# Kernel tuning notes

Hardware: AMD Instinct MI355X
Metric: run time of the kernel (lower is better)

## Reference

```python
import jax, jax.numpy as jnp
import numpy as np
import math

BATCH, DIM, T, WIDTH = 4096, 100, 101, 200

def setup_inputs() -> dict:
    key = jax.random.key(0)
    ks = jax.random.split(key, 12)
    def lin(k, nin, nout):
        bound = 1.0 / math.sqrt(nin)
        kw, kb = jax.random.split(k)
        W = jax.random.uniform(kw, (nin, nout), jnp.float32, -bound, bound)
        b = jax.random.uniform(kb, (nout,), jnp.float32, -bound, bound)
        return W, b
    W0, b0 = lin(ks[0], DIM + 1, WIDTH)
    W1, b1 = lin(ks[1], WIDTH, WIDTH)
    W2, b2 = lin(ks[2], WIDTH, WIDTH)
    W3, b3 = lin(ks[3], WIDTH, WIDTH)
    Wout, bout = lin(ks[4], WIDTH, DIM)
    S0 = jax.random.normal(ks[5], (BATCH, DIM), jnp.float32)
    # standard-normal increments; scaled by sqrt(h) inside reference (matches torch randn * sqrt(h))
    dW = jax.random.normal(ks[6], (BATCH, DIM * T), jnp.float32)
    timegrid = jnp.linspace(0.0, 1.0, T, dtype=jnp.float32)
    return {"S0": S0, "timegrid": timegrid, "dW": dW,
            "W0": W0, "b0": b0, "W1": W1, "b1": b1, "W2": W2, "b2": b2,
            "W3": W3, "b3": b3, "Wout": Wout, "bout": bout}

def _mlp(x, W0, b0, W1, b1, W2, b2, W3, b3, Wout, bout):
    h = jax.nn.relu(x @ W0 + b0)
    h = jax.nn.relu(h @ W1 + b1)
    h = jax.nn.relu(h @ W2 + b2)
    h = jax.nn.relu(h @ W3 + b3)
    return h @ Wout + bout

def reference(S0, timegrid, dW, W0, b0, W1, b1, W2, b2, W3, b3, Wout, bout):
    B, dim = S0.shape
    T_ = timegrid.shape[0]
    h = timegrid[1] - timegrid[0]
    # [B, T*dim] -> [T-1, B, dim]: slices (i-1)*dim:i*dim for i=1..T-1
    dWs = jnp.sqrt(h) * jnp.transpose(dW.reshape(B, T_, dim)[:, :T_ - 1], (1, 0, 2))
    ts = timegrid[:T_ - 1]  # t_{i-1} for i = 1..T-1

    def step(carry, xs):
        S, err = carry
        t, dWi = xs
        inp = jnp.concatenate([jnp.broadcast_to(t, (B, 1)), S], axis=1)
        u = _mlp(inp, W0, b0, W1, b1, W2, b2, W3, b3, Wout, bout)
        err = err + (u * u) * h          # ff_fun running cost
        S = S + u * h + u * dWi          # drift b_fun=u, diffusion sigma_fun=u
        return (S, err), None

    (S_final, err), _ = jax.lax.scan(step, (S0, jnp.zeros_like(S0)), (ts, dWs))
    return err + S_final * S_final       # terminal cost g_fun(x,u)=x*x
```

## Files before the change

### kernel.cpp

```cpp
#include <hip/hip_runtime.h>


typedef __attribute__((ext_vector_type(8))) short  bf16x8;
typedef __attribute__((ext_vector_type(4))) float  f32x4;

#define MFMA16(A,B,C) __builtin_amdgcn_mfma_f32_16x16x32_bf16((A),(B),(C),0,0,0)

#define NBATCH 4096
#define NDIM   100
#define NT     101
#define NWID   200

#define E0   (13*4*512)
#define E1   (13*7*512)
#define EOUTW (7*7*512)
#define OFF0 0
#define OFF1 (E0)
#define OFF2 (OFF1+E1)
#define OFF3 (OFF2+E1)
#define OFF4 (OFF3+E1)
#define TOTE (OFF4+EOUTW)

__device__ __forceinline__ unsigned short f2bf(float x){
  unsigned u = __float_as_uint(x);
  unsigned r = (u + 0x7fffu + ((u >> 16) & 1u)) >> 16;
  return (unsigned short)r;
}

__device__ __forceinline__ bf16x8 zero8(){
  bf16x8 z;
#pragma unroll
  for (int e = 0; e < 8; ++e) z[e] = 0;
  return z;
}

__device__ __forceinline__ void st_act(unsigned short* buf, int m, int k, unsigned short v){
  buf[(((k >> 5) * 64) + (((k >> 3) & 3) * 16) + m) * 8 + (k & 7)] = v;
}

__global__ void pack_w(const float* __restrict__ W0, const float* __restrict__ W1,
                       const float* __restrict__ W2, const float* __restrict__ W3,
                       const float* __restrict__ Wo, unsigned short* __restrict__ out){
  int idx = blockIdx.x * 256 + threadIdx.x;
  if (idx >= TOTE) return;
  const float* src; int Kt, Nt, KI, local;
  if      (idx < OFF1){ src = W0; Kt = 101; Nt = 200; KI = 4; local = idx - OFF0; }
  else if (idx < OFF2){ src = W1; Kt = 200; Nt = 200; KI = 7; local = idx - OFF1; }
  else if (idx < OFF3){ src = W2; Kt = 200; Nt = 200; KI = 7; local = idx - OFF2; }
  else if (idx < OFF4){ src = W3; Kt = 200; Nt = 200; KI = 7; local = idx - OFF3; }
  else                { src = Wo; Kt = 200; Nt = 100; KI = 7; local = idx - OFF4; }
  int per_tile = KI * 512;
  int tile = local / per_tile;
  int rem  = local - tile * per_tile;
  int kit  = rem >> 9;
  int within = rem & 511;
  int lane = within >> 3, j = within & 7;
  int n = tile * 16 + (lane & 15);
  int k = kit * 32 + (lane >> 4) * 8 + j;
  unsigned short v = 0;
  if (k < Kt && n < Nt) v = f2bf(src[k * Nt + n]);
  out[idx] = v;
}

__global__ __launch_bounds__(512, 2) void solver(
    const float* __restrict__ S0,  const float* __restrict__ tg,
    const float* __restrict__ dW,  const unsigned short* __restrict__ Wp,
    const float* __restrict__ b0g, const float* __restrict__ b1g,
    const float* __restrict__ b2g, const float* __restrict__ b3g,
    const float* __restrict__ bog, float* __restrict__ outp)
{
  __shared__ unsigned short sm_t0[2048];
  __shared__ unsigned short sm_a[3584];
  __shared__ unsigned short sm_b[3584];
  __shared__ float sbias[944];
  float* sb0 = sbias;       float* sb1 = sbias + 208;
  float* sb2 = sbias + 416; float* sb3 = sbias + 624;
  float* sbo = sbias + 832;

  const int tid  = threadIdx.x;
  const int lane = tid & 63;
  const int w    = tid >> 6;
  const int q    = lane >> 4;
  const int mr   = lane & 15;
  const int blk  = blockIdx.x;
  const bool t1ok = (w < 5);
  const bool act4 = (w < 7);

  for (int i = tid; i < 1024; i += 512) ((unsigned*)sm_t0)[i] = 0u;
  for (int i = tid; i < 1792; i += 512) ((unsigned*)sm_a )[i] = 0u;
  for (int i = tid; i < 1792; i += 512) ((unsigned*)sm_b )[i] = 0u;
  for (int i = tid; i < 208; i += 512){
    float z0 = (i < 200) ? b0g[i] : 0.f; sb0[i] = z0;
    float z1 = (i < 200) ? b1g[i] : 0.f; sb1[i] = z1;
    float z2 = (i < 200) ? b2g[i] : 0.f; sb2[i] = z2;
    float z3 = (i < 200) ? b3g[i] : 0.f; sb3[i] = z3;
  }
  for (int i = tid; i < 112; i += 512) sbo[i] = (i < 100) ? bog[i] : 0.f;

  bf16x8 w1f[2][7], w2f[2][7], w3f[2][7], wo_f[7];
#pragma unroll
  for (int k = 0; k < 7; ++k){
    w1f[0][k] = *(const bf16x8*)(Wp + OFF1 + ((w * 7 + k) * 64 + lane) * 8);
    w2f[0][k] = *(const bf16x8*)(Wp + OFF2 + ((w * 7 + k) * 64 + lane) * 8);
    w3f[0][k] = *(const bf16x8*)(Wp + OFF3 + ((w * 7 + k) * 64 + lane) * 8);
    if (t1ok){
      w1f[1][k] = *(const bf16x8*)(Wp + OFF1 + (((w + 8) * 7 + k) * 64 + lane) * 8);
      w2f[1][k] = *(const bf16x8*)(Wp + OFF2 + (((w + 8) * 7 + k) * 64 + lane) * 8);
      w3f[1][k] = *(const bf16x8*)(Wp + OFF3 + (((w + 8) * 7 + k) * 64 + lane) * 8);
    } else {
      w1f[1][k] = zero8(); w2f[1][k] = zero8(); w3f[1][k] = zero8();
    }
    wo_f[k] = act4 ? *(const bf16x8*)(Wp + OFF4 + ((w * 7 + k) * 64 + lane) * 8)
                   : zero8();
  }

  const int cc  = w * 16 + mr;
  const bool cok = act4 && (cc < 100);
  float Sr[4], Er[4];
#pragma unroll
  for (int i = 0; i < 4; ++i){
    int b = blk * 16 + q * 4 + i;
    Sr[i] = cok ? S0[b * NDIM + cc] : 0.f;
    Er[i] = 0.f;
  }
  if (act4){
#pragma unroll
    for (int i = 0; i < 4; ++i)
      st_act(sm_t0, q * 4 + i, 1 + cc, f2bf(Sr[i]));
  }

  const float hh = tg[1] - tg[0];
  const float sq = sqrtf(hh);

#define HIDDEN_LAYER(SRC, DST, WF, SB)                                        \
  { f32x4 accA = {0.f,0.f,0.f,0.f}, accB = {0.f,0.f,0.f,0.f};                 \
    _Pragma("unroll")                                                         \
    for (int k = 0; k < 7; ++k){                                              \
      bf16x8 a = *(const bf16x8*)((SRC) + (k * 64 + lane) * 8);               \
      accA = MFMA16(a, WF[0][k], accA);                                       \
      if (t1ok) accB = MFMA16(a, WF[1][k], accB);                             \
    }                                                                         \
    { int c0 = w * 16 + mr;                                                   \
      _Pragma("unroll")                                                       \
      for (int i = 0; i < 4; ++i){                                            \
        float v = accA[i] + SB[c0]; v = fmaxf(v, 0.f);                        \
        st_act(DST, q * 4 + i, c0, f2bf(v)); } }                              \
    if (t1ok){ int c1 = (w + 8) * 16 + mr;                                    \
      _Pragma("unroll")                                                       \
      for (int i = 0; i < 4; ++i){                                            \
        float v = accB[i] + SB[c1]; v = fmaxf(v, 0.f);                        \
        st_act(DST, q * 4 + i, c1, f2bf(v)); } }                              \
  }

  for (int t = 0; t < 100; ++t){
    if (tid < 16) sm_t0[tid * 8] = f2bf(tg[t]);
    float dwr[4];
#pragma unroll
    for (int i = 0; i < 4; ++i){
      int b = blk * 16 + q * 4 + i;
      int d = cok ? cc : 0;
      dwr[i] = act4 ? dW[b * 10100 + t * 100 + d] : 0.f;
    }
    __syncthreads();

    {
      f32x4 acc0 = {0.f,0.f,0.f,0.f}, acc1 = {0.f,0.f,0.f,0.f};
#pragma unroll
      for (int k = 0; k < 4; ++k){
        bf16x8 a  = *(const bf16x8*)(sm_t0 + (k * 64 + lane) * 8);
        bf16x8 bA = *(const bf16x8*)(Wp + OFF0 + ((w * 4 + k) * 64 + lane) * 8);
        acc0 = MFMA16(a, bA, acc0);
        if (t1ok){
          bf16x8 bB = *(const bf16x8*)(Wp + OFF0 + (((w + 8) * 4 + k) * 64 + lane) * 8);
          acc1 = MFMA16(a, bB, acc1);
        }
      }
      { int c0 = w * 16 + mr;
#pragma unroll
        for (int i = 0; i < 4; ++i){
          float v = acc0[i] + sb0[c0]; v = fmaxf(v, 0.f);
          st_act(sm_a, q * 4 + i, c0, f2bf(v)); } }
      if (t1ok){ int c1 = (w + 8) * 16 + mr;
#pragma unroll
        for (int i = 0; i < 4; ++i){
          float v = acc1[i] + sb0[c1]; v = fmaxf(v, 0.f);
          st_act(sm_a, q * 4 + i, c1, f2bf(v)); } }
    }
    __syncthreads();
    HIDDEN_LAYER(sm_a, sm_b, w1f, sb1)
    __syncthreads();
    HIDDEN_LAYER(sm_b, sm_a, w2f, sb2)
    __syncthreads();
    HIDDEN_LAYER(sm_a, sm_b, w3f, sb3)
    __syncthreads();

    if (act4){
      f32x4 a4 = {0.f,0.f,0.f,0.f};
#pragma unroll
      for (int k = 0; k < 7; ++k){
        bf16x8 a = *(const bf16x8*)(sm_b + (k * 64 + lane) * 8);
        a4 = MFMA16(a, wo_f[k], a4);
      }
#pragma unroll
      for (int i = 0; i < 4; ++i){
        float u = a4[i] + sbo[cc];
        Er[i] += u * u * hh;
        Sr[i] += u * (hh + sq * dwr[i]);
        st_act(sm_t0, q * 4 + i, 1 + cc, f2bf(Sr[i]));
      }
    }
  }

  if (cok){
#pragma unroll
    for (int i = 0; i < 4; ++i){
      int b = blk * 16 + q * 4 + i;
      outp[b * NDIM + cc] = Er[i] + Sr[i] * Sr[i];
    }
  }
#undef HIDDEN_LAYER
}

extern "C" void kernel_launch(void* const* d_in, const int* in_sizes, int n_in,
                              void* d_out, int out_size, void* d_ws, size_t ws_size,
                              hipStream_t stream) {
  const float* S0  = (const float*)d_in[0];
  const float* tg  = (const float*)d_in[1];
  const float* dW  = (const float*)d_in[2];
  const float* W0  = (const float*)d_in[3];
  const float* b0  = (const float*)d_in[4];
  const float* W1  = (const float*)d_in[5];
  const float* b1  = (const float*)d_in[6];
  const float* W2  = (const float*)d_in[7];
  const float* b2  = (const float*)d_in[8];
  const float* W3  = (const float*)d_in[9];
  const float* b3  = (const float*)d_in[10];
  const float* Wo  = (const float*)d_in[11];
  const float* bo  = (const float*)d_in[12];
  unsigned short* Wp = (unsigned short*)d_ws;

  pack_w<<<(TOTE + 255) / 256, 256, 0, stream>>>(W0, W1, W2, W3, Wo, Wp);
  solver<<<256, 512, 0, stream>>>(S0, tg, dW, Wp, b0, b1, b2, b3, bo, (float*)d_out);
}
```

Before: 552.8 us.

## Fold biases into weights, transpose MFMA operands, stage W0 in LDS

Folds every bias into the packed weight matrices as an extra K row, with a constant-one column in the activation buffers, so the per-layer bias loads from shared memory go away. MFMA operands are swapped so each lane writes four contiguous features per row with one packed 8-byte store into padded row-major LDS buffers, replacing scattered 2-byte stores. W0 is copied into LDS once instead of being read from global memory on every timestep. The change also vectorises the dW, S0 and output accesses and prefetches the next time value. The cost is about 53KB more shared memory per block, which may limit occupancy, plus a larger fixed layout that could bring bank conflicts.

Result: faster. 456.2 us (-17.5%).

```diff
diff --git a/kernel.cpp b/kernel.cpp
--- a/kernel.cpp
+++ b/kernel.cpp
@@ -6,76 +6,65 @@
 
 #define MFMA16(A,B,C) __builtin_amdgcn_mfma_f32_16x16x32_bf16((A),(B),(C),0,0,0)
 
-#define NBATCH 4096
-#define NDIM   100
-#define NT     101
-#define NWID   200
-
-#define E0   (13*4*512)
-#define E1   (13*7*512)
-#define EOUTW (7*7*512)
-#define OFF0 0
-#define OFF1 (E0)
+#define FS 232
+
+#define OFF1 26624
+#define E1   46592
 #define OFF2 (OFF1+E1)
 #define OFF3 (OFF2+E1)
 #define OFF4 (OFF3+E1)
-#define TOTE (OFF4+EOUTW)
+#define TOTE (OFF4+7*7*512)
 
 __device__ __forceinline__ unsigned short f2bf(float x){
   unsigned u = __float_as_uint(x);
-  unsigned r = (u + 0x7fffu + ((u >> 16) & 1u)) >> 16;
-  return (unsigned short)r;
-}
-
-__device__ __forceinline__ bf16x8 zero8(){
-  bf16x8 z;
-#pragma unroll
-  for (int e = 0; e < 8; ++e) z[e] = 0;
-  return z;
-}
-
-__device__ __forceinline__ void st_act(unsigned short* buf, int m, int k, unsigned short v){
-  buf[(((k >> 5) * 64) + (((k >> 3) & 3) * 16) + m) * 8 + (k & 7)] = v;
-}
-
-__global__ void pack_w(const float* __restrict__ W0, const float* __restrict__ W1,
-                       const float* __restrict__ W2, const float* __restrict__ W3,
-                       const float* __restrict__ Wo, unsigned short* __restrict__ out){
+  return (unsigned short)((u + 0x7fffu + ((u >> 16) & 1u)) >> 16);
+}
+
+__global__ void pack_w(const float* __restrict__ W0, const float* __restrict__ b0,
+                       const float* __restrict__ W1, const float* __restrict__ b1,
+                       const float* __restrict__ W2, const float* __restrict__ b2,
+                       const float* __restrict__ W3, const float* __restrict__ b3,
+                       const float* __restrict__ Wo, const float* __restrict__ bo,
+                       unsigned short* __restrict__ out){
   int idx = blockIdx.x * 256 + threadIdx.x;
   if (idx >= TOTE) return;
-  const float* src; int Kt, Nt, KI, local;
-  if      (idx < OFF1){ src = W0; Kt = 101; Nt = 200; KI = 4; local = idx - OFF0; }
-  else if (idx < OFF2){ src = W1; Kt = 200; Nt = 200; KI = 7; local = idx - OFF1; }
-  else if (idx < OFF3){ src = W2; Kt = 200; Nt = 200; KI = 7; local = idx - OFF2; }
-  else if (idx < OFF4){ src = W3; Kt = 200; Nt = 200; KI = 7; local = idx - OFF3; }
-  else                { src = Wo; Kt = 200; Nt = 100; KI = 7; local = idx - OFF4; }
+  const float *Ws, *bs; int KI, NT, local, isw0 = 0;
+  if      (idx < OFF1){ Ws = W0; bs = b0; KI = 4; NT = 200; local = idx;        isw0 = 1; }
+  else if (idx < OFF2){ Ws = W1; bs = b1; KI = 7; NT = 200; local = idx - OFF1; }
+  else if (idx < OFF3){ Ws = W2; bs = b2; KI = 7; NT = 200; local = idx - OFF2; }
+  else if (idx < OFF4){ Ws = W3; bs = b3; KI = 7; NT = 200; local = idx - OFF3; }
+  else                { Ws = Wo; bs = bo; KI = 7; NT = 100; local = idx - OFF4; }
   int per_tile = KI * 512;
   int tile = local / per_tile;
   int rem  = local - tile * per_tile;
   int kit  = rem >> 9;
   int within = rem & 511;
-  int lane = within >> 3, j = within & 7;
-  int n = tile * 16 + (lane & 15);
-  int k = kit * 32 + (lane >> 4) * 8 + j;
-  unsigned short v = 0;
-  if (k < Kt && n < Nt) v = f2bf(src[k * Nt + n]);
-  out[idx] = v;
-}
-
-__global__ __launch_bounds__(512, 2) void solver(
-    const float* __restrict__ S0,  const float* __restrict__ tg,
-    const float* __restrict__ dW,  const unsigned short* __restrict__ Wp,
-    const float* __restrict__ b0g, const float* __restrict__ b1g,
-    const float* __restrict__ b2g, const float* __restrict__ b3g,
-    const float* __restrict__ bog, float* __restrict__ outp)
+  int ln = within >> 3, j = within & 7;
+  int n = tile * 16 + (ln & 15);
+  int k = kit * 32 + (ln >> 4) * 8 + j;
+  float v = 0.f;
+  if (n < NT){
+    if (isw0){
+      if      (k < 100)  v = Ws[(1 + k) * 200 + n];
+      else if (k == 100) v = Ws[n];
+      else if (k == 101) v = bs[n];
+    } else {
+      if      (k < 200)  v = Ws[k * NT + n];
+      else if (k == 200) v = bs[n];
+    }
+  }
+  out[idx] = f2bf(v);
+}
+
+__global__ __launch_bounds__(512, 2) __attribute__((amdgpu_waves_per_eu(2, 2)))
+void solver(const float* __restrict__ S0, const float* __restrict__ tg,
+            const float* __restrict__ dW, const unsigned short* __restrict__ Wp,
+            float* __restrict__ outp)
 {
-  __shared__ unsigned short sm_t0[2048];
-  __shared__ unsigned short sm_a[3584];
-  __shared__ unsigned short sm_b[3584];
-  __shared__ float sbias[944];
-  float* sb0 = sbias;       float* sb1 = sbias + 208;
-  float* sb2 = sbias + 416; float* sb3 = sbias + 624;
-  float* sbo = sbias + 832;
+  __shared__ __attribute__((aligned(16))) unsigned short sW0[26624];
+  __shared__ __attribute__((aligned(16))) unsigned short sIn[16 * FS];
+  __shared__ __attribute__((aligned(16))) unsigned short sA [16 * FS];
+  __shared__ __attribute__((aligned(16))) unsigned short sB [16 * FS];
 
   const int tid  = threadIdx.x;
   const int lane = tid & 63;
@@ -83,162 +72,168 @@
   const int q    = lane >> 4;
   const int mr   = lane & 15;
   const int blk  = blockIdx.x;
-  const bool t1ok = (w < 5);
-  const bool act4 = (w < 7);
-
-  for (int i = tid; i < 1024; i += 512) ((unsigned*)sm_t0)[i] = 0u;
-  for (int i = tid; i < 1792; i += 512) ((unsigned*)sm_a )[i] = 0u;
-  for (int i = tid; i < 1792; i += 512) ((unsigned*)sm_b )[i] = 0u;
-  for (int i = tid; i < 208; i += 512){
-    float z0 = (i < 200) ? b0g[i] : 0.f; sb0[i] = z0;
-    float z1 = (i < 200) ? b1g[i] : 0.f; sb1[i] = z1;
-    float z2 = (i < 200) ? b2g[i] : 0.f; sb2[i] = z2;
-    float z3 = (i < 200) ? b3g[i] : 0.f; sb3[i] = z3;
-  }
-  for (int i = tid; i < 112; i += 512) sbo[i] = (i < 100) ? bog[i] : 0.f;
+  const bool has2   = (w < 5);
+  const bool hasOut = (w < 7);
+  const int t0 = w, t1 = w + 8;
+  const int f0 = w * 16 + q * 4;
+  const bool fvalid = hasOut && (f0 <= 96);
+  const int rowoff = mr * FS;
+
+  for (int i = tid; i < 16 * FS / 2; i += 512){
+    ((unsigned*)sIn)[i] = 0u; ((unsigned*)sA)[i] = 0u; ((unsigned*)sB)[i] = 0u;
+  }
+  for (int i = tid; i < 3328; i += 512)
+    ((uint4*)sW0)[i] = ((const uint4*)Wp)[i];
+  if (tid < 16){
+    sIn[tid * FS + 101] = 0x3F80;
+    sA [tid * FS + 200] = 0x3F80;
+    sB [tid * FS + 200] = 0x3F80;
+  }
 
   bf16x8 w1f[2][7], w2f[2][7], w3f[2][7], wo_f[7];
 #pragma unroll
   for (int k = 0; k < 7; ++k){
-    w1f[0][k] = *(const bf16x8*)(Wp + OFF1 + ((w * 7 + k) * 64 + lane) * 8);
-    w2f[0][k] = *(const bf16x8*)(Wp + OFF2 + ((w * 7 + k) * 64 + lane) * 8);
-    w3f[0][k] = *(const bf16x8*)(Wp + OFF3 + ((w * 7 + k) * 64 + lane) * 8);
-    if (t1ok){
-      w1f[1][k] = *(const bf16x8*)(Wp + OFF1 + (((w + 8) * 7 + k) * 64 + lane) * 8);
-      w2f[1][k] = *(const bf16x8*)(Wp + OFF2 + (((w + 8) * 7 + k) * 64 + lane) * 8);
-      w3f[1][k] = *(const bf16x8*)(Wp + OFF3 + (((w + 8) * 7 + k) * 64 + lane) * 8);
-    } else {
-      w1f[1][k] = zero8(); w2f[1][k] = zero8(); w3f[1][k] = zero8();
-    }
-    wo_f[k] = act4 ? *(const bf16x8*)(Wp + OFF4 + ((w * 7 + k) * 64 + lane) * 8)
-                   : zero8();
-  }
-
-  const int cc  = w * 16 + mr;
-  const bool cok = act4 && (cc < 100);
-  float Sr[4], Er[4];
-#pragma unroll
-  for (int i = 0; i < 4; ++i){
-    int b = blk * 16 + q * 4 + i;
-    Sr[i] = cok ? S0[b * NDIM + cc] : 0.f;
-    Er[i] = 0.f;
-  }
-  if (act4){
-#pragma unroll
-    for (int i = 0; i < 4; ++i)
-      st_act(sm_t0, q * 4 + i, 1 + cc, f2bf(Sr[i]));
+    w1f[0][k] = *(const bf16x8*)(Wp + OFF1 + ((t0 * 7 + k) * 64 + lane) * 8);
+    w2f[0][k] = *(const bf16x8*)(Wp + OFF2 + ((t0 * 7 + k) * 64 + lane) * 8);
+    w3f[0][k] = *(const bf16x8*)(Wp + OFF3 + ((t0 * 7 + k) * 64 + lane) * 8);
+  }
+  if (has2){
+#pragma unroll
+    for (int k = 0; k < 7; ++k){
+      w1f[1][k] = *(const bf16x8*)(Wp + OFF1 + ((t1 * 7 + k) * 64 + lane) * 8);
+      w2f[1][k] = *(const bf16x8*)(Wp + OFF2 + ((t1 * 7 + k) * 64 + lane) * 8);
+      w3f[1][k] = *(const bf16x8*)(Wp + OFF3 + ((t1 * 7 + k) * 64 + lane) * 8);
+    }
+  }
+  if (hasOut){
+#pragma unroll
+    for (int k = 0; k < 7; ++k)
+      wo_f[k] = *(const bf16x8*)(Wp + OFF4 + ((w * 7 + k) * 64 + lane) * 8);
+  }
+
+  float Sr[4] = {0.f, 0.f, 0.f, 0.f}, Er[4] = {0.f, 0.f, 0.f, 0.f};
+  if (fvalid){
+    f32x4 s0v = *(const f32x4*)(S0 + (blk * 16 + mr) * 100 + f0);
+#pragma unroll
+    for (int i = 0; i < 4; ++i) Sr[i] = s0v[i];
+    unsigned lo = (unsigned)f2bf(Sr[0]) | ((unsigned)f2bf(Sr[1]) << 16);
+    unsigned hi = (unsigned)f2bf(Sr[2]) | ((unsigned)f2bf(Sr[3]) << 16);
+    uint2 pp; pp.x = lo; pp.y = hi;
+    *(uint2*)&sIn[rowoff + f0] = pp;
   }
 
   const float hh = tg[1] - tg[0];
   const float sq = sqrtf(hh);
-
-#define HIDDEN_LAYER(SRC, DST, WF, SB)                                        \
-  { f32x4 accA = {0.f,0.f,0.f,0.f}, accB = {0.f,0.f,0.f,0.f};                 \
+  float tcur = tg[0];
+
+#define EPI(DST, TL, ACC) {                                                   \
+    int ff = (TL) * 16 + q * 4;                                               \
+    if (!((TL) == 12 && q >= 2)){                                             \
+      float v0 = fmaxf((ACC)[0], 0.f), v1 = fmaxf((ACC)[1], 0.f);             \
+      float v2 = fmaxf((ACC)[2], 0.f), v3 = fmaxf((ACC)[3], 0.f);             \
+      unsigned lo = (unsigned)f2bf(v0) | ((unsigned)f2bf(v1) << 16);          \
+      unsigned hi = (unsigned)f2bf(v2) | ((unsigned)f2bf(v3) << 16);          \
+      uint2 pp; pp.x = lo; pp.y = hi;                                         \
+      *(uint2*)&(DST)[rowoff + ff] = pp;                                      \
+    } }
+
+#define HIDDEN(SRC, DST, WF) {                                                \
+    f32x4 acc0 = {0.f,0.f,0.f,0.f}, acc1 = {0.f,0.f,0.f,0.f};                 \
     _Pragma("unroll")                                                         \
     for (int k = 0; k < 7; ++k){                                              \
-      bf16x8 a = *(const bf16x8*)((SRC) + (k * 64 + lane) * 8);               \
-      accA = MFMA16(a, WF[0][k], accA);                                       \
-      if (t1ok) accB = MFMA16(a, WF[1][k], accB);                             \
+      bf16x8 b = *(const bf16x8*)((SRC) + rowoff + k * 32 + q * 8);           \
+      acc0 = MFMA16(WF[0][k], b, acc0);                                       \
+      if (has2) acc1 = MFMA16(WF[1][k], b, acc1);                             \
     }                                                                         \
-    { int c0 = w * 16 + mr;                                                   \
-      _Pragma("unroll")                                                       \
-      for (int i = 0; i < 4; ++i){                                            \
-        float v = accA[i] + SB[c0]; v = fmaxf(v, 0.f);                        \
-        st_act(DST, q * 4 + i, c0, f2bf(v)); } }                              \
-    if (t1ok){ int c1 = (w + 8) * 16 + mr;                                    \
-      _Pragma("unroll")                                                       \
-      for (int i = 0; i < 4; ++i){                                            \
-        float v = accB[i] + SB[c1]; v = fmaxf(v, 0.f);                        \
-        st_act(DST, q * 4 + i, c1, f2bf(v)); } }                              \
-  }
+    EPI(DST, t0, acc0)                                                        \
+    if (has2) EPI(DST, t1, acc1)                                              \
+  }
+
+  __syncthreads();
 
   for (int t = 0; t < 100; ++t){
-    if (tid < 16) sm_t0[tid * 8] = f2bf(tg[t]);
-    float dwr[4];
-#pragma unroll
-    for (int i = 0; i < 4; ++i){
-      int b = blk * 16 + q * 4 + i;
-      int d = cok ? cc : 0;
-      dwr[i] = act4 ? dW[b * 10100 + t * 100 + d] : 0.f;
-    }
+    f32x4 dwf = {0.f, 0.f, 0.f, 0.f};
+    if (fvalid)
+      dwf = *(const f32x4*)(dW + (blk * 16 + mr) * 10100 + t * 100 + f0);
+    if (tid < 16) sIn[tid * FS + 100] = f2bf(tcur);
+    float tnext = tg[t + 1];
     __syncthreads();
 
     {
       f32x4 acc0 = {0.f,0.f,0.f,0.f}, acc1 = {0.f,0.f,0.f,0.f};
 #pragma unroll
       for (int k = 0; k < 4; ++k){
-        bf16x8 a  = *(const bf16x8*)(sm_t0 + (k * 64 + lane) * 8);
-        bf16x8 bA = *(const bf16x8*)(Wp + OFF0 + ((w * 4 + k) * 64 + lane) * 8);
-        acc0 = MFMA16(a, bA, acc0);
-        if (t1ok){
-          bf16x8 bB = *(const bf16x8*)(Wp + OFF0 + (((w + 8) * 4 + k) * 64 + lane) * 8);
-          acc1 = MFMA16(a, bB, acc1);
+        bf16x8 b  = *(const bf16x8*)(sIn + rowoff + k * 32 + q * 8);
+        bf16x8 a0 = *(const bf16x8*)(sW0 + ((t0 * 4 + k) * 64 + lane) * 8);
+        acc0 = MFMA16(a0, b, acc0);
+        if (has2){
+          bf16x8 a1 = *(const bf16x8*)(sW0 + ((t1 * 4 + k) * 64 + lane) * 8);
+          acc1 = MFMA16(a1, b, acc1);
         }
       }
-      { int c0 = w * 16 + mr;
+      EPI(sA, t0, acc0)
+      if (has2) EPI(sA, t1, acc1)
+    }
+    __syncthreads();
+    HIDDEN(sA, sB, w1f)
+    __syncthreads();
+    HIDDEN(sB, sA, w2f)
+    __syncthreads();
+    HIDDEN(sA, sB, w3f)
+    __syncthreads();
+
+    if (hasOut){
+      f32x4 a4 = {0.f, 0.f, 0.f, 0.f};
+#pragma unroll
+      for (int k = 0; k < 7; ++k){
+        bf16x8 b = *(const bf16x8*)(sB + rowoff + k * 32 + q * 8);
+        a4 = MFMA16(wo_f[k], b, a4);
+      }
+      if (fvalid){
 #pragma unroll
         for (int i = 0; i < 4; ++i){
-          float v = acc0[i] + sb0[c0]; v = fmaxf(v, 0.f);
-          st_act(sm_a, q * 4 + i, c0, f2bf(v)); } }
-      if (t1ok){ int c1 = (w + 8) * 16 + mr;
-#pragma unroll
-        for (int i = 0; i < 4; ++i){
-          float v = acc1[i] + sb0[c1]; v = fmaxf(v, 0.f);
-          st_act(sm_a, q * 4 + i, c1, f2bf(v)); } }
-    }
-    __syncthreads();
-    HIDDEN_LAYER(sm_a, sm_b, w1f, sb1)
-    __syncthreads();
-    HIDDEN_LAYER(sm_b, sm_a, w2f, sb2)
-    __syncthreads();
-    HIDDEN_LAYER(sm_a, sm_b, w3f, sb3)
-    __syncthreads();
-
-    if (act4){
-      f32x4 a4 = {0.f,0.f,0.f,0.f};
-#pragma unroll
-      for (int k = 0; k < 7; ++k){
-        bf16x8 a = *(const bf16x8*)(sm_b + (k * 64 + lane) * 8);
-        a4 = MFMA16(a, wo_f[k], a4);
+          float u = a4[i];
+          Er[i] += u * u * hh;
+          Sr[i] += u * (hh + sq * dwf[i]);
+        }
+        unsigned lo = (unsigned)f2bf(Sr[0]) | ((unsigned)f2bf(Sr[1]) << 16);
+        unsigned hi = (unsigned)f2bf(Sr[2]) | ((unsigned)f2bf(Sr[3]) << 16);
+        uint2 pp; pp.x = lo; pp.y = hi;
+        *(uint2*)&sIn[rowoff + f0] = pp;
       }
-#pragma unroll
-      for (int i = 0; i < 4; ++i){
-        float u = a4[i] + sbo[cc];
-        Er[i] += u * u * hh;
-        Sr[i] += u * (hh + sq * dwr[i]);
-        st_act(sm_t0, q * 4 + i, 1 + cc, f2bf(Sr[i]));
-      }
-    }
-  }
-
-  if (cok){
-#pragma unroll
-    for (int i = 0; i < 4; ++i){
-      int b = blk * 16 + q * 4 + i;
-      outp[b * NDIM + cc] = Er[i] + Sr[i] * Sr[i];
-    }
-  }
-#undef HIDDEN_LAYER
+    }
+    tcur = tnext;
+  }
+
+  if (fvalid){
+    f32x4 o;
+#pragma unroll
+    for (int i = 0; i < 4; ++i) o[i] = Er[i] + Sr[i] * Sr[i];
+    *(f32x4*)(outp + (blk * 16 + mr) * 100 + f0) = o;
+  }
+#undef HIDDEN
+#undef EPI
 }
 
 extern "C" void kernel_launch(void* const* d_in, const int* in_sizes, int n_in,
                               void* d_out, int out_size, void* d_ws, size_t ws_size,
                               hipStream_t stream) {
-  const float* S0  = (const float*)d_in[0];
-  const float* tg  = (const float*)d_in[1];
-  const float* dW  = (const float*)d_in[2];
-  const float* W0  = (const float*)d_in[3];
-  const float* b0  = (const float*)d_in[4];
-  const float* W1  = (const float*)d_in[5];
-  const float* b1  = (const float*)d_in[6];
-  const float* W2  = (const float*)d_in[7];
-  const float* b2  = (const float*)d_in[8];
-  const float* W3  = (const float*)d_in[9];
-  const float* b3  = (const float*)d_in[10];
-  const float* Wo  = (const float*)d_in[11];
-  const float* bo  = (const float*)d_in[12];
+  const float* S0 = (const float*)d_in[0];
+  const float* tg = (const float*)d_in[1];
+  const float* dW = (const float*)d_in[2];
+  const float* W0 = (const float*)d_in[3];
+  const float* b0 = (const float*)d_in[4];
+  const float* W1 = (const float*)d_in[5];
+  const float* b1 = (const float*)d_in[6];
+  const float* W2 = (const float*)d_in[7];
+  const float* b2 = (const float*)d_in[8];
+  const float* W3 = (const float*)d_in[9];
+  const float* b3 = (const float*)d_in[10];
+  const float* Wo = (const float*)d_in[11];
+  const float* bo = (const float*)d_in[12];
   unsigned short* Wp = (unsigned short*)d_ws;
 
-  pack_w<<<(TOTE + 255) / 256, 256, 0, stream>>>(W0, W1, W2, W3, Wo, Wp);
-  solver<<<256, 512, 0, stream>>>(S0, tg, dW, Wp, b0, b1, b2, b3, bo, (float*)d_out);
-}
+  pack_w<<<(TOTE + 255) / 256, 256, 0, stream>>>(W0, b0, W1, b1, W2, b2, W3, b3,
+                                                 Wo, bo, Wp);
+  solver<<<256, 512, 0, stream>>>(S0, tg, dW, Wp, (float*)d_out);
+}
```
